# Kernel tuning notes

Measured on AMD Instinct MI355X. Metric: run time of the kernel, lower is better.

Reference implementation:

```python
import jax, jax.numpy as jnp
import numpy as np

T, N, C, RADIUS = 64, 16, 256, 64
D_OUT = 2 * RADIUS + 1
TAU = 2.0
DECAY = float(np.exp(-1.0 / TAU))  # first-order leaky (LIF) filter decay
WEIGHT0 = 6.53543197272069


def setup_inputs() -> dict:
    key = jax.random.key(0)
    k1, k2 = jax.random.split(key)
    inp = jax.random.uniform(k1, (T, N, C, 2), dtype=jnp.float32)
    delay_param = jnp.arange(-RADIUS, RADIUS + 1, dtype=jnp.float32)[:, None]  # (D_out, 1)
    weight = jnp.asarray(WEIGHT0, dtype=jnp.float32)
    u = jax.random.uniform(k2, (N, C, D_OUT, 2), dtype=jnp.float32)  # bernoulli uniforms
    return {"input": inp, "delay_param": delay_param, "weight": weight, "u": u}


def reference(input, delay_param, weight, u):
    Tn, Nn, Cn, _ = input.shape
    # delay = relu(cat([_delay, -_delay], dim=1))  -> (D_out, 2), nonnegative
    delay = jax.nn.relu(jnp.concatenate([delay_param, -delay_param], axis=1))
    Do = delay.shape[0]
    # input.unsqueeze(-2).repeat(..., D_out, 1) -> (T, N, C, D_out, 2)
    x = jnp.broadcast_to(input[:, :, :, None, :], (Tn, Nn, Cn, Do, 2))
    # stochastic rounding of per-synapse delay
    bd = jnp.broadcast_to(delay[None, None], (Nn, Cn, Do, 2))
    df = jnp.floor(bd)
    rounded = jnp.where(u < bd - df, df + 1.0, df)
    # clamp so the (one-hot) spike at argmax(t) stays inside the window
    spike_t = jnp.argmax(x, axis=0)  # (N, C, D_out, 2)
    rounded = jnp.minimum(rounded, (Tn - 1 - spike_t).astype(rounded.dtype))
    d = rounded.astype(jnp.int32)
    # circular shift along time: out[t] = x[(t - d) % T]
    t_idx = jnp.arange(Tn)[:, None, None, None, None]
    idx = (t_idx - d[None]) % Tn
    shifted = jnp.take_along_axis(x, idx, axis=0)  # (T, N, C, D_out, 2)
    # LIF filter (leaky integrator over time, state reset at t=0)
    def step(v, xt):
        v = v * DECAY + xt
        return v, v
    _, filt = jax.lax.scan(step, jnp.zeros_like(shifted[0]), shifted)
    # scale by fixed synaptic weight and sum over the 2 input channels
    return jnp.sum(filt * weight, axis=-1)  # (T, N, C, D_out)
```

## Files before the change

kernel.cpp:

```cpp
#include <hip/hip_runtime.h>
#include <hip/hip_bf16.h>

#define T_DIM 64
#define NP 4096
#define D_OUTC 129

__global__ __launch_bounds__(256, 8) void jeffress_kernel(
    const float* __restrict__ input,
    const float* __restrict__ delay_param,
    const float* __restrict__ weight,
    const float* __restrict__ u,
    float* __restrict__ out)
{
    __shared__ float x_lds[2][64];
    __shared__ __hip_bfloat16 G[2][64 * 64];
    __shared__ int shifts[D_OUTC];
    __shared__ int cap[2];

    const int p   = blockIdx.x;
    const int tid = threadIdx.x;
    const float DECAY = 0.6065306597126334f;

    if (tid < 128) {
        int ch = tid >> 6, t = tid & 63;
        float xv = input[(t * NP + p) * 2 + ch];
        x_lds[ch][t] = xv;
        unsigned b = __float_as_uint(xv);
        b ^= (b & 0x80000000u) ? 0xffffffffu : 0x80000000u;
        unsigned long long key = ((unsigned long long)b << 32) | (unsigned)(63 - t);
        #pragma unroll
        for (int m = 1; m < 64; m <<= 1) {
            unsigned long long o = __shfl_xor(key, m, 64);
            if (o > key) key = o;
        }
        if ((tid & 63) == 0) cap[ch] = (int)(key & 0xffffffffull);
    }
    __syncthreads();

    if (tid < 128) {
        int ch = tid >> 6, s = tid & 63;
        const float* xs = x_lds[ch];
        __hip_bfloat16* g = G[ch];
        float v = 0.0f;
        #pragma unroll 4
        for (int t = 0; t < 64; ++t) {
            v = v * DECAY + xs[(t - s) & 63];
            g[t * 64 + s] = __float2bfloat16(v);
        }
    } else {
        int c0 = cap[0], c1 = cap[1];
        for (int d = tid - 128; d < D_OUTC; d += 128) {
            float dp = delay_param[d];
            float b0 = fmaxf(dp, 0.0f), b1 = fmaxf(-dp, 0.0f);
            float2 uu = ((const float2*)u)[p * D_OUTC + d];
            float f0 = floorf(b0), f1 = floorf(b1);
            float r0 = (uu.x < b0 - f0) ? f0 + 1.0f : f0;
            float r1 = (uu.y < b1 - f1) ? f1 + 1.0f : f1;
            int s0 = (int)fminf(r0, (float)c0);
            int s1 = (int)fminf(r1, (float)c1);
            shifts[d] = s0 | (s1 << 16);
        }
    }
    __syncthreads();

    const float w = weight[0];
    int d = (tid < D_OUTC) ? tid : tid - D_OUTC;
    int t = (tid < D_OUTC) ? 0 : 1;
    const __hip_bfloat16* G0 = G[0];
    const __hip_bfloat16* G1 = G[1];
    while (t < T_DIM) {
        int sp = shifts[d];
        int s0 = sp & 0xffff, s1 = sp >> 16;
        float v = __bfloat162float(G0[t * 64 + s0]) + __bfloat162float(G1[t * 64 + s1]);
        out[(t * NP + p) * D_OUTC + d] = w * v;
        d += 127; t += 1;
        if (d >= D_OUTC) { d -= D_OUTC; ++t; }
    }
}

extern "C" void kernel_launch(void* const* d_in, const int* in_sizes, int n_in,
                              void* d_out, int out_size, void* d_ws, size_t ws_size,
                              hipStream_t stream) {
    const float* input       = (const float*)d_in[0];
    const float* delay_param = (const float*)d_in[1];
    const float* weight      = (const float*)d_in[2];
    const float* u           = (const float*)d_in[3];
    float* out = (float*)d_out;

    jeffress_kernel<<<NP, 256, 0, stream>>>(input, delay_param, weight, u, out);
}
```

Baseline: 165.1 us.

## Compute per-delay LIF scan directly instead of precomputed bf16 shift table

Drops the shared-memory bf16 table of filtered signals for every shift. Each thread now owns one delay output and runs the leaky-integrator recurrence over a doubled input buffer, which removes the bf16 rounding and the extra barrier phase. Block size is halved to 128 with one thread doing a second delay column, and block indices are swizzled across positions. In exchange, each thread does a serial 64-step dependent FMA chain, and the store pattern is now one column per thread at every time step.

```diff
diff --git a/kernel.cpp b/kernel.cpp
--- a/kernel.cpp
+++ b/kernel.cpp
@@ -1,80 +1,82 @@
 #include <hip/hip_runtime.h>
-#include <hip/hip_bf16.h>
 
 #define T_DIM 64
 #define NP 4096
 #define D_OUTC 129
+#define ROW_STRIDE (NP * D_OUTC)
 
-__global__ __launch_bounds__(256, 8) void jeffress_kernel(
+__global__ __launch_bounds__(128, 8) void jeffress_kernel(
     const float* __restrict__ input,
     const float* __restrict__ delay_param,
     const float* __restrict__ weight,
     const float* __restrict__ u,
     float* __restrict__ out)
 {
-    __shared__ float x_lds[2][64];
-    __shared__ __hip_bfloat16 G[2][64 * 64];
-    __shared__ int shifts[D_OUTC];
-    __shared__ int cap[2];
+    __shared__ float x_lds[2][128];
+    __shared__ int caps[2];
 
-    const int p   = blockIdx.x;
-    const int tid = threadIdx.x;
+    const int p    = ((blockIdx.x & 7) << 9) | (blockIdx.x >> 3);
+    const int tid  = threadIdx.x;
+    const int lane = tid & 63, wave = tid >> 6;
     const float DECAY = 0.6065306597126334f;
 
-    if (tid < 128) {
-        int ch = tid >> 6, t = tid & 63;
-        float xv = input[(t * NP + p) * 2 + ch];
-        x_lds[ch][t] = xv;
+    {
+        float xv = input[(lane * NP + p) * 2 + wave];
+        x_lds[wave][lane]      = xv;
+        x_lds[wave][lane + 64] = xv;
         unsigned b = __float_as_uint(xv);
         b ^= (b & 0x80000000u) ? 0xffffffffu : 0x80000000u;
-        unsigned long long key = ((unsigned long long)b << 32) | (unsigned)(63 - t);
+        unsigned long long key = ((unsigned long long)b << 32) | (unsigned)(63 - lane);
         #pragma unroll
-        for (int m = 1; m < 64; m <<= 1) {
-            unsigned long long o = __shfl_xor(key, m, 64);
+        for (int mm = 1; mm < 64; mm <<= 1) {
+            unsigned long long o = __shfl_xor(key, mm, 64);
             if (o > key) key = o;
         }
-        if ((tid & 63) == 0) cap[ch] = (int)(key & 0xffffffffull);
+        if (lane == 0) caps[wave] = (int)(key & 0xffffffffull);
     }
     __syncthreads();
 
-    if (tid < 128) {
-        int ch = tid >> 6, s = tid & 63;
-        const float* xs = x_lds[ch];
-        __hip_bfloat16* g = G[ch];
-        float v = 0.0f;
-        #pragma unroll 4
-        for (int t = 0; t < 64; ++t) {
-            v = v * DECAY + xs[(t - s) & 63];
-            g[t * 64 + s] = __float2bfloat16(v);
+    const float w   = weight[0];
+    const float c0f = (float)caps[0], c1f = (float)caps[1];
+
+    const int d     = (wave << 6) | lane;
+    const bool dual = (tid == 127);
+
+    auto calc = [&](int dd, int& s0, int& s1) {
+        float dp = delay_param[dd];
+        float b0 = fmaxf(dp, 0.0f), b1 = fmaxf(-dp, 0.0f);
+        float2 uu = ((const float2*)u)[p * D_OUTC + dd];
+        float f0 = floorf(b0), f1 = floorf(b1);
+        float r0 = (uu.x < b0 - f0) ? f0 + 1.0f : f0;
+        float r1 = (uu.y < b1 - f1) ? f1 + 1.0f : f1;
+        s0 = (int)fminf(r0, c0f);
+        s1 = (int)fminf(r1, c1f);
+    };
+
+    int s0, s1;
+    calc(d, s0, s1);
+    int e0 = 0, e1 = 0;
+    if (dual) calc(128, e0, e1);
+
+    const float* x0 = &x_lds[0][64 - s0];
+    const float* x1 = &x_lds[1][64 - s1];
+    const float* y0 = &x_lds[0][64 - e0];
+    const float* y1 = &x_lds[1][64 - e1];
+
+    float v0 = 0.0f, v1 = 0.0f, ve0 = 0.0f, ve1 = 0.0f;
+    float* rp = out + (size_t)p * D_OUTC + d;
+
+    #pragma unroll 4
+    for (int t = 0; t < T_DIM; ++t) {
+        v0 = v0 * DECAY + x0[t];
+        v1 = v1 * DECAY + x1[t];
+        rp[0] = w * (v0 + v1);
+        if (dual) {
+            ve0 = ve0 * DECAY + y0[t];
+            ve1 = ve1 * DECAY + y1[t];
+            rp[1] = w * (ve0 + ve1);
         }
-    } else {
-        int c0 = cap[0], c1 = cap[1];
-        for (int d = tid - 128; d < D_OUTC; d += 128) {
-            float dp = delay_param[d];
-            float b0 = fmaxf(dp, 0.0f), b1 = fmaxf(-dp, 0.0f);
-            float2 uu = ((const float2*)u)[p * D_OUTC + d];
-            float f0 = floorf(b0), f1 = floorf(b1);
-            float r0 = (uu.x < b0 - f0) ? f0 + 1.0f : f0;
-            float r1 = (uu.y < b1 - f1) ? f1 + 1.0f : f1;
-            int s0 = (int)fminf(r0, (float)c0);
-            int s1 = (int)fminf(r1, (float)c1);
-            shifts[d] = s0 | (s1 << 16);
-        }
-    }
-    __syncthreads();
-
-    const float w = weight[0];
-    int d = (tid < D_OUTC) ? tid : tid - D_OUTC;
-    int t = (tid < D_OUTC) ? 0 : 1;
-    const __hip_bfloat16* G0 = G[0];
-    const __hip_bfloat16* G1 = G[1];
-    while (t < T_DIM) {
-        int sp = shifts[d];
-        int s0 = sp & 0xffff, s1 = sp >> 16;
-        float v = __bfloat162float(G0[t * 64 + s0]) + __bfloat162float(G1[t * 64 + s1]);
-        out[(t * NP + p) * D_OUTC + d] = w * v;
-        d += 127; t += 1;
-        if (d >= D_OUTC) { d -= D_OUTC; ++t; }
+        rp += ROW_STRIDE;
     }
 }
 
@@ -87,5 +89,5 @@
     const float* u           = (const float*)d_in[3];
     float* out = (float*)d_out;
 
-    jeffress_kernel<<<NP, 256, 0, stream>>>(input, delay_param, weight, u, out);
+    jeffress_kernel<<<NP, 128, 0, stream>>>(input, delay_param, weight, u, out);
 }
```

After: 163.2 us. Within noise of the previous version (-1.1%).
